# Performance work log

Hardware: AMD Instinct MI355X
Metric: run time of the kernel (lower is better)

The kernel has to match this reference:

```python
import jax, jax.numpy as jnp
import numpy as np

NUM_VARS = 64
EDGE_TYPES = 4
HID = 128
IN = 32
BATCH = 64
SKIP_FIRST = True


def setup_inputs() -> dict:
    key = jax.random.key(0)
    ks = jax.random.split(key, 16)
    adj = np.ones((NUM_VARS, NUM_VARS)) - np.eye(NUM_VARS)
    send, recv = np.where(adj)  # [N*(N-1)] each
    E = send.shape[0]
    s = 0.05
    return {
        'inputs': jax.random.normal(ks[0], (BATCH, NUM_VARS, IN), jnp.float32),
        'edges': jax.random.uniform(ks[1], (BATCH, E, EDGE_TYPES), dtype=jnp.float32),
        'msg_fc1_w': jax.random.normal(ks[2], (EDGE_TYPES, HID, 2 * IN), jnp.float32) * s,
        'msg_fc1_b': jax.random.normal(ks[3], (EDGE_TYPES, HID), jnp.float32) * s,
        'msg_fc2_w': jax.random.normal(ks[4], (EDGE_TYPES, HID, HID), jnp.float32) * s,
        'msg_fc2_b': jax.random.normal(ks[5], (EDGE_TYPES, HID), jnp.float32) * s,
        'out_fc1_w': jax.random.normal(ks[6], (HID, IN + HID), jnp.float32) * s,
        'out_fc1_b': jax.random.normal(ks[7], (HID,), jnp.float32) * s,
        'out_fc2_w': jax.random.normal(ks[8], (HID, HID), jnp.float32) * s,
        'out_fc2_b': jax.random.normal(ks[9], (HID,), jnp.float32) * s,
        'mu_w': jax.random.normal(ks[10], (IN, HID), jnp.float32) * s,
        'mu_b': jax.random.normal(ks[11], (IN,), jnp.float32) * s,
        'logstd_w': jax.random.normal(ks[12], (IN, HID), jnp.float32) * s,
        'logstd_b': jax.random.normal(ks[13], (IN,), jnp.float32) * s,
        'send_edges': jnp.asarray(send, jnp.int32),
        'recv_edges': jnp.asarray(recv, jnp.int32),
    }


def reference(inputs, edges, msg_fc1_w, msg_fc1_b, msg_fc2_w, msg_fc2_b,
              out_fc1_w, out_fc1_b, out_fc2_w, out_fc2_b,
              mu_w, mu_b, logstd_w, logstd_b, send_edges, recv_edges):
    # gather receiver/sender node features per edge: [B, E, 2*D]
    receivers = inputs[:, recv_edges, :]
    senders = inputs[:, send_edges, :]
    pre_msg = jnp.concatenate([receivers, senders], axis=-1)
    B, E, _ = pre_msg.shape
    all_msgs = jnp.zeros((B, E, HID), pre_msg.dtype)
    start = 1 if SKIP_FIRST else 0
    for i in range(start, EDGE_TYPES):  # small fixed loop over structurally distinct MLPs
        m = jax.nn.relu(jnp.einsum('bej,hj->beh', pre_msg, msg_fc1_w[i]) + msg_fc1_b[i])
        m = jax.nn.relu(jnp.einsum('beh,oh->beo', m, msg_fc2_w[i]) + msg_fc2_b[i])
        all_msgs = all_msgs + m * edges[:, :, i:i + 1]
    # scatter-add messages to receiver nodes (replaces dense one-hot matmul)
    agg_msgs = jnp.zeros((B, NUM_VARS, HID), all_msgs.dtype).at[:, recv_edges, :].add(all_msgs)
    aug_inputs = jnp.concatenate([inputs, agg_msgs], axis=-1)
    pred = jax.nn.relu(aug_inputs @ out_fc1_w.T + out_fc1_b)
    pred = jax.nn.relu(pred @ out_fc2_w.T + out_fc2_b)
    mu = pred @ mu_w.T + mu_b
    log_std = jnp.clip(pred @ logstd_w.T + logstd_b, -3.0, 1.0)
    std = jnp.exp(log_std)  # eval mode: std_gating = 0, noise suppressed
    pred_out = mu  # mu + 0 * noise * std
    return inputs + pred_out
```

## Files before the change

### kernel.cpp

```cpp
#include <hip/hip_runtime.h>
#include <hip/hip_bf16.h>

#define B_ 64
#define V_ 64
#define E_ 4032
#define HID_ 128
#define IN_ 32

typedef __attribute__((ext_vector_type(8))) __bf16 bf16x8;
typedef __attribute__((ext_vector_type(4))) __bf16 bf16x4;
typedef __attribute__((ext_vector_type(4))) float f32x4;

__global__ void __launch_bounds__(256) node_h1(
    const float* __restrict__ x, const float* __restrict__ w1,
    const float* __restrict__ b1, float* __restrict__ h1r,
    float* __restrict__ h1s) {
  const int bid = blockIdx.x, t = threadIdx.x;
  const int h = t & 127, half = t >> 7;
  __shared__ float xs[2][IN_];
  if (t < 64) xs[t >> 5][t & 31] = x[bid * 64 + t];
  __syncthreads();
#pragma unroll
  for (int tt = 0; tt < 3; ++tt) {
    const float* wrow = w1 + ((size_t)((tt + 1) * HID_ + h)) * (2 * IN_) + half * IN_;
    float4 w[8];
#pragma unroll
    for (int j = 0; j < 8; ++j) w[j] = ((const float4*)wrow)[j];
    const float bias = half ? 0.f : b1[(tt + 1) * HID_ + h];
    float* dst = (half ? h1s : h1r) + ((size_t)tt * (B_ * V_) + bid * 2) * HID_ + h;
#pragma unroll
    for (int n = 0; n < 2; ++n) {
      float acc = bias;
#pragma unroll
      for (int j = 0; j < 8; ++j)
        acc += w[j].x * xs[n][4 * j] + w[j].y * xs[n][4 * j + 1] +
               w[j].z * xs[n][4 * j + 2] + w[j].w * xs[n][4 * j + 3];
      dst[n * HID_] = acc;
    }
  }
}

__global__ void __launch_bounds__(256) weight_prep(
    const float* __restrict__ w2, const float* __restrict__ fc1w,
    const float* __restrict__ fc2w, const float* __restrict__ muw,
    unsigned short* __restrict__ w2f, float* __restrict__ fc1wT,
    float* __restrict__ fc2wT, float* __restrict__ muwT) {
  const int i = blockIdx.x * 256 + threadIdx.x;
  if (i < 49152) {
    const int e = i & 7, lane = (i >> 3) & 63, ks = (i >> 9) & 3;
    const int nt = (i >> 11) & 1, w = (i >> 12) & 3, tt = i >> 14;
    const int o = w * 32 + nt * 16 + (lane & 15);
    const int k = ks * 32 + (lane >> 4) * 8 + e;
    w2f[i] = __builtin_bit_cast(unsigned short,
                                (__bf16)w2[((size_t)((tt + 1) * HID_ + o)) * HID_ + k]);
    return;
  }
  int j = i - 49152;
  if (j < 20480) { fc1wT[j] = fc1w[(j & 127) * (IN_ + HID_) + (j >> 7)]; return; }
  j -= 20480;
  if (j < 16384) { fc2wT[j] = fc2w[(j & 127) * HID_ + (j >> 7)]; return; }
  j -= 16384;
  if (j < 4096) { muwT[j] = muw[(j & 31) * HID_ + (j >> 5)]; }
}

__global__ void __launch_bounds__(256)
edge_mfma(const float* __restrict__ edges, const float* __restrict__ b2,
          const float* __restrict__ h1r, const float* __restrict__ h1s,
          const unsigned short* __restrict__ w2f, float* __restrict__ aggout) {
  const int v = blockIdx.x, b = blockIdx.y, t = threadIdx.x;
  const int wave = t >> 6, lane = t & 63;
  const int l15 = lane & 15, lg = lane >> 4;
  const int kq = lane & 31, rpar = lane >> 5;

  __shared__ __align__(16) unsigned short m1[2][64 * HID_];
  __shared__ float ew[3 * 64];

  if (wave < 3) {
    float wgt = 0.f;
    if (lane < 63) {
      const int uu = (lane < v) ? lane : lane + 1;
      const int eg = uu * 63 + ((v > uu) ? (v - 1) : v);
      wgt = edges[(b * E_ + eg) * 4 + wave + 1];
    }
    ew[wave * 64 + lane] = wgt;
  }

  {
    float4 hr = *(const float4*)(h1r + ((size_t)b * V_ + v) * HID_ + kq * 4);
#pragma unroll
    for (int j = 0; j < 8; ++j) {
      const int r = wave * 16 + j * 2 + rpar;
      int u = (r < v) ? r : r + 1;
      if (r == 63) u = v;
      float4 hs = *(const float4*)(h1s + ((size_t)b * V_ + u) * HID_ + kq * 4);
      bf16x4 pk;
      pk[0] = (__bf16)fmaxf(hr.x + hs.x, 0.f);
      pk[1] = (__bf16)fmaxf(hr.y + hs.y, 0.f);
      pk[2] = (__bf16)fmaxf(hr.z + hs.z, 0.f);
      pk[3] = (__bf16)fmaxf(hr.w + hs.w, 0.f);
      *(bf16x4*)((char*)m1[0] + r * 256 + ((kq * 8) ^ ((r & 7) << 4))) = pk;
    }
  }

  bf16x8 bfrag[2][4];
  float b2r[2];
#pragma unroll
  for (int nt = 0; nt < 2; ++nt) {
#pragma unroll
    for (int ks = 0; ks < 4; ++ks)
      bfrag[nt][ks] = *(const bf16x8*)(w2f + (((wave * 2 + nt) * 4 + ks) * 64 + lane) * 8);
    b2r[nt] = b2[HID_ + wave * 32 + nt * 16 + l15];
  }

  float acc[4][2][4];
#pragma unroll
  for (int mt = 0; mt < 4; ++mt)
#pragma unroll
    for (int nt = 0; nt < 2; ++nt)
#pragma unroll
      for (int r = 0; r < 4; ++r) acc[mt][nt][r] = 0.f;

  __syncthreads();

#pragma unroll
  for (int tt = 0; tt < 3; ++tt) {
    float4 hrn, hsn[8];
    if (tt < 2) {
      hrn = *(const float4*)(h1r + ((size_t)((tt + 1) * B_ + b) * V_ + v) * HID_ + kq * 4);
#pragma unroll
      for (int j = 0; j < 8; ++j) {
        const int r = wave * 16 + j * 2 + rpar;
        int u = (r < v) ? r : r + 1;
        if (r == 63) u = v;
        hsn[j] = *(const float4*)(h1s + ((size_t)((tt + 1) * B_ + b) * V_ + u) * HID_ + kq * 4);
      }
    }
    const unsigned short* mb = m1[tt & 1];
#pragma unroll
    for (int mt = 0; mt < 4; ++mt) {
      bf16x8 af[4];
#pragma unroll
      for (int ks = 0; ks < 4; ++ks) {
        const int row = mt * 16 + l15;
        af[ks] = *(const bf16x8*)((const char*)mb + row * 256 +
                                  ((ks * 64 + lg * 16) ^ ((row & 7) << 4)));
      }
#pragma unroll
      for (int nt = 0; nt < 2; ++nt) {
        f32x4 macc = {0.f, 0.f, 0.f, 0.f};
#pragma unroll
        for (int ks = 0; ks < 4; ++ks)
          macc = __builtin_amdgcn_mfma_f32_16x16x32_bf16(af[ks], bfrag[nt][ks], macc, 0, 0, 0);
#pragma unroll
        for (int r = 0; r < 4; ++r)
          acc[mt][nt][r] += fmaxf(macc[r] + b2r[nt], 0.f) * ew[tt * 64 + mt * 16 + lg * 4 + r];
      }
    }
    if (tt < 2) {
#pragma unroll
      for (int j = 0; j < 8; ++j) {
        const int r = wave * 16 + j * 2 + rpar;
        bf16x4 pk;
        pk[0] = (__bf16)fmaxf(hrn.x + hsn[j].x, 0.f);
        pk[1] = (__bf16)fmaxf(hrn.y + hsn[j].y, 0.f);
        pk[2] = (__bf16)fmaxf(hrn.z + hsn[j].z, 0.f);
        pk[3] = (__bf16)fmaxf(hrn.w + hsn[j].w, 0.f);
        *(bf16x4*)((char*)m1[(tt + 1) & 1] + r * 256 + ((kq * 8) ^ ((r & 7) << 4))) = pk;
      }
#pragma unroll
      for (int nt = 0; nt < 2; ++nt) {
#pragma unroll
        for (int ks = 0; ks < 4; ++ks)
          bfrag[nt][ks] = *(const bf16x8*)(
              w2f + (((((tt + 1) * 4 + wave) * 2 + nt) * 4 + ks) * 64 + lane) * 8);
        b2r[nt] = b2[(tt + 2) * HID_ + wave * 32 + nt * 16 + l15];
      }
    }
    __syncthreads();
  }

#pragma unroll
  for (int nt = 0; nt < 2; ++nt) {
    float s = 0.f;
#pragma unroll
    for (int mt = 0; mt < 4; ++mt)
#pragma unroll
      for (int r = 0; r < 4; ++r) s += acc[mt][nt][r];
    s += __shfl_xor(s, 16);
    s += __shfl_xor(s, 32);
    if (lane < 16)
      aggout[((size_t)b * V_ + v) * HID_ + wave * 32 + nt * 16 + l15] = s;
  }
}

__global__ void __launch_bounds__(256) out_mlp(
    const float* __restrict__ x, const float* __restrict__ aggout,
    const float* __restrict__ fc1wT, const float* __restrict__ fc1b,
    const float* __restrict__ fc2wT, const float* __restrict__ fc2b,
    const float* __restrict__ muwT, const float* __restrict__ mub,
    float* __restrict__ out) {
  const int t = threadIdx.x;
  const int g = t >> 5, j = t & 31;
  const int nodebase = blockIdx.x * 8;
  __shared__ float aug[8][160];
  __shared__ float p1[8][HID_];
  __shared__ float p2[8][HID_];

  aug[t >> 5][t & 31] = x[nodebase * IN_ + t];
  {
    float4 a4 = *(const float4*)(aggout + (size_t)nodebase * HID_ + t * 4);
    *(float4*)&aug[t >> 5][IN_ + (t & 31) * 4] = a4;
  }
  __syncthreads();

  float4 a1 = *(const float4*)(fc1b + j * 4);
#pragma unroll 4
  for (int k = 0; k < IN_ + HID_; ++k) {
    float4 w = *(const float4*)(fc1wT + (size_t)k * HID_ + j * 4);
    const float a = aug[g][k];
    a1.x += w.x * a; a1.y += w.y * a; a1.z += w.z * a; a1.w += w.w * a;
  }
  a1.x = fmaxf(a1.x, 0.f); a1.y = fmaxf(a1.y, 0.f);
  a1.z = fmaxf(a1.z, 0.f); a1.w = fmaxf(a1.w, 0.f);
  *(float4*)&p1[g][j * 4] = a1;
  __syncthreads();

  float4 a2 = *(const float4*)(fc2b + j * 4);
#pragma unroll 4
  for (int k = 0; k < HID_; ++k) {
    float4 w = *(const float4*)(fc2wT + (size_t)k * HID_ + j * 4);
    const float a = p1[g][k];
    a2.x += w.x * a; a2.y += w.y * a; a2.z += w.z * a; a2.w += w.w * a;
  }
  a2.x = fmaxf(a2.x, 0.f); a2.y = fmaxf(a2.y, 0.f);
  a2.z = fmaxf(a2.z, 0.f); a2.w = fmaxf(a2.w, 0.f);
  *(float4*)&p2[g][j * 4] = a2;
  __syncthreads();

  float am = mub[j];
#pragma unroll 4
  for (int k = 0; k < HID_; ++k) am += muwT[k * IN_ + j] * p2[g][k];
  out[(size_t)(nodebase + g) * IN_ + j] = aug[g][j] + am;
}

extern "C" void kernel_launch(void* const* d_in, const int* in_sizes, int n_in,
                              void* d_out, int out_size, void* d_ws, size_t ws_size,
                              hipStream_t stream) {
  const float* x     = (const float*)d_in[0];
  const float* edges = (const float*)d_in[1];
  const float* w1    = (const float*)d_in[2];
  const float* b1    = (const float*)d_in[3];
  const float* w2    = (const float*)d_in[4];
  const float* b2    = (const float*)d_in[5];
  const float* fc1w  = (const float*)d_in[6];
  const float* fc1b  = (const float*)d_in[7];
  const float* fc2w  = (const float*)d_in[8];
  const float* fc2b  = (const float*)d_in[9];
  const float* muw   = (const float*)d_in[10];
  const float* mub   = (const float*)d_in[11];
  float* out = (float*)d_out;

  float* h1r    = (float*)d_ws;
  float* h1s    = h1r + 3 * (B_ * V_) * HID_;
  float* aggout = h1s + 3 * (B_ * V_) * HID_;
  float* fc1wT  = aggout + (B_ * V_) * HID_;
  float* fc2wT  = fc1wT + (IN_ + HID_) * HID_;
  float* muwT   = fc2wT + HID_ * HID_;
  unsigned short* w2f = (unsigned short*)(muwT + HID_ * IN_);

  node_h1<<<2048, 256, 0, stream>>>(x, w1, b1, h1r, h1s);
  weight_prep<<<352, 256, 0, stream>>>(w2, fc1w, fc2w, muw, w2f, fc1wT, fc2wT, muwT);
  edge_mfma<<<dim3(V_, B_), 256, 0, stream>>>(edges, b2, h1r, h1s, w2f, aggout);
  out_mlp<<<512, 256, 0, stream>>>(x, aggout, fc1wT, fc1b, fc2wT, fc2b, muwT, mub, out);
}
```

Before: 185.9 us.

## Store node projections in fp16, merge prep kernels, pre-transpose edge weights

Node hidden projections h1r/h1s are now stored as fp16 instead of fp32, which halves the gather traffic in the edge kernel. The relu-add is done with packed half math, and the MFMA switches from bf16 to the f16 variant. The two prep kernels are merged into one launch, which also writes a per-(b,v) transposed edge-weight table so the edge kernel does one contiguous load instead of strided gathers. The out_mlp shared arrays are padded. This trades an extra workspace buffer and fp16 range/precision risk for less memory traffic and launch overhead.

```diff
diff --git a/kernel.cpp b/kernel.cpp
--- a/kernel.cpp
+++ b/kernel.cpp
@@ -1,114 +1,132 @@
 #include <hip/hip_runtime.h>
 #include <hip/hip_bf16.h>
+#include <hip/hip_fp16.h>
 
 #define B_ 64
 #define V_ 64
 #define E_ 4032
 #define HID_ 128
 #define IN_ 32
-
-typedef __attribute__((ext_vector_type(8))) __bf16 bf16x8;
-typedef __attribute__((ext_vector_type(4))) __bf16 bf16x4;
+#define BV_ (B_ * V_)
+
+typedef __attribute__((ext_vector_type(2))) _Float16 f16x2;
+typedef __attribute__((ext_vector_type(8))) _Float16 f16x8;
 typedef __attribute__((ext_vector_type(4))) float f32x4;
 
-__global__ void __launch_bounds__(256) node_h1(
+__device__ __forceinline__ f16x2 bc2(unsigned u) { return __builtin_bit_cast(f16x2, u); }
+__device__ __forceinline__ unsigned bcu(f16x2 h) { return __builtin_bit_cast(unsigned, h); }
+
+__global__ void __launch_bounds__(256) prep_all(
     const float* __restrict__ x, const float* __restrict__ w1,
-    const float* __restrict__ b1, float* __restrict__ h1r,
-    float* __restrict__ h1s) {
+    const float* __restrict__ b1, const float* __restrict__ w2,
+    const float* __restrict__ edges, const float* __restrict__ fc1w,
+    const float* __restrict__ fc2w, const float* __restrict__ muw,
+    _Float16* __restrict__ h1r, _Float16* __restrict__ h1s,
+    _Float16* __restrict__ w2f, float* __restrict__ ewT,
+    float* __restrict__ fc1wT, float* __restrict__ fc2wT,
+    float* __restrict__ muwT) {
   const int bid = blockIdx.x, t = threadIdx.x;
-  const int h = t & 127, half = t >> 7;
-  __shared__ float xs[2][IN_];
-  if (t < 64) xs[t >> 5][t & 31] = x[bid * 64 + t];
-  __syncthreads();
-#pragma unroll
-  for (int tt = 0; tt < 3; ++tt) {
-    const float* wrow = w1 + ((size_t)((tt + 1) * HID_ + h)) * (2 * IN_) + half * IN_;
-    float4 w[8];
-#pragma unroll
-    for (int j = 0; j < 8; ++j) w[j] = ((const float4*)wrow)[j];
-    const float bias = half ? 0.f : b1[(tt + 1) * HID_ + h];
-    float* dst = (half ? h1s : h1r) + ((size_t)tt * (B_ * V_) + bid * 2) * HID_ + h;
-#pragma unroll
-    for (int n = 0; n < 2; ++n) {
-      float acc = bias;
-#pragma unroll
-      for (int j = 0; j < 8; ++j)
-        acc += w[j].x * xs[n][4 * j] + w[j].y * xs[n][4 * j + 1] +
-               w[j].z * xs[n][4 * j + 2] + w[j].w * xs[n][4 * j + 3];
-      dst[n * HID_] = acc;
-    }
-  }
-}
-
-__global__ void __launch_bounds__(256) weight_prep(
-    const float* __restrict__ w2, const float* __restrict__ fc1w,
-    const float* __restrict__ fc2w, const float* __restrict__ muw,
-    unsigned short* __restrict__ w2f, float* __restrict__ fc1wT,
-    float* __restrict__ fc2wT, float* __restrict__ muwT) {
-  const int i = blockIdx.x * 256 + threadIdx.x;
-  if (i < 49152) {
+
+  if (bid < 2048) {
+    __shared__ float xs[2][IN_];
+    if (t < 64) xs[t >> 5][t & 31] = x[bid * 64 + t];
+    __syncthreads();
+    const int h = t & 127, half_ = t >> 7;
+#pragma unroll
+    for (int tt = 0; tt < 3; ++tt) {
+      const float* wrow = w1 + ((size_t)((tt + 1) * HID_ + h)) * (2 * IN_) + half_ * IN_;
+      float4 w[8];
+#pragma unroll
+      for (int j = 0; j < 8; ++j) w[j] = ((const float4*)wrow)[j];
+      const float bias = half_ ? 0.f : b1[(tt + 1) * HID_ + h];
+      _Float16* dst = (half_ ? h1s : h1r) + ((size_t)tt * BV_ + bid * 2) * HID_ + h;
+#pragma unroll
+      for (int n = 0; n < 2; ++n) {
+        float acc = bias;
+#pragma unroll
+        for (int j = 0; j < 8; ++j)
+          acc += w[j].x * xs[n][4 * j] + w[j].y * xs[n][4 * j + 1] +
+                 w[j].z * xs[n][4 * j + 2] + w[j].w * xs[n][4 * j + 3];
+        dst[n * HID_] = (_Float16)acc;
+      }
+    }
+    return;
+  }
+  if (bid < 2240) {
+    const int i = (bid - 2048) * 256 + t;
     const int e = i & 7, lane = (i >> 3) & 63, ks = (i >> 9) & 3;
     const int nt = (i >> 11) & 1, w = (i >> 12) & 3, tt = i >> 14;
     const int o = w * 32 + nt * 16 + (lane & 15);
     const int k = ks * 32 + (lane >> 4) * 8 + e;
-    w2f[i] = __builtin_bit_cast(unsigned short,
-                                (__bf16)w2[((size_t)((tt + 1) * HID_ + o)) * HID_ + k]);
-    return;
-  }
-  int j = i - 49152;
-  if (j < 20480) { fc1wT[j] = fc1w[(j & 127) * (IN_ + HID_) + (j >> 7)]; return; }
-  j -= 20480;
-  if (j < 16384) { fc2wT[j] = fc2w[(j & 127) * HID_ + (j >> 7)]; return; }
-  j -= 16384;
-  if (j < 4096) { muwT[j] = muw[(j & 31) * HID_ + (j >> 5)]; }
+    w2f[i] = (_Float16)w2[((size_t)((tt + 1) * HID_ + o)) * HID_ + k];
+    return;
+  }
+  if (bid < 2400) {
+    int j = (bid - 2240) * 256 + t;
+    if (j < 20480) { fc1wT[j] = fc1w[(j & 127) * (IN_ + HID_) + (j >> 7)]; return; }
+    j -= 20480;
+    if (j < 16384) { fc2wT[j] = fc2w[(j & 127) * HID_ + (j >> 7)]; return; }
+    j -= 16384;
+    muwT[j] = muw[(j & 31) * HID_ + (j >> 5)];
+    return;
+  }
+  {
+    const int g = bid - 2400;
+    if (t < 192) {
+      const int b = g >> 6, v = g & 63;
+      const int tt = t >> 6, r = t & 63;
+      float val = 0.f;
+      if (r < 63) {
+        const int u = (r < v) ? r : r + 1;
+        const int vv = (v > u) ? v - 1 : v;
+        val = edges[((size_t)b * E_ + u * 63 + vv) * 4 + tt + 1];
+      }
+      ewT[(size_t)g * 192 + t] = val;
+    }
+    return;
+  }
 }
 
 __global__ void __launch_bounds__(256)
-edge_mfma(const float* __restrict__ edges, const float* __restrict__ b2,
-          const float* __restrict__ h1r, const float* __restrict__ h1s,
-          const unsigned short* __restrict__ w2f, float* __restrict__ aggout) {
+edge_mfma(const float* __restrict__ b2, const _Float16* __restrict__ h1r,
+          const _Float16* __restrict__ h1s, const _Float16* __restrict__ w2f,
+          const float* __restrict__ ewT, float* __restrict__ aggout) {
   const int v = blockIdx.x, b = blockIdx.y, t = threadIdx.x;
   const int wave = t >> 6, lane = t & 63;
   const int l15 = lane & 15, lg = lane >> 4;
   const int kq = lane & 31, rpar = lane >> 5;
 
   __shared__ __align__(16) unsigned short m1[2][64 * HID_];
-  __shared__ float ew[3 * 64];
-
-  if (wave < 3) {
-    float wgt = 0.f;
-    if (lane < 63) {
-      const int uu = (lane < v) ? lane : lane + 1;
-      const int eg = uu * 63 + ((v > uu) ? (v - 1) : v);
-      wgt = edges[(b * E_ + eg) * 4 + wave + 1];
-    }
-    ew[wave * 64 + lane] = wgt;
-  }
+  __shared__ __align__(16) float ews[192];
+
+  if (t < 192) ews[t] = ewT[((size_t)b * V_ + v) * 192 + t];
 
   {
-    float4 hr = *(const float4*)(h1r + ((size_t)b * V_ + v) * HID_ + kq * 4);
+    const unsigned short* hrp =
+        (const unsigned short*)h1r + ((size_t)b * V_ + v) * HID_ + kq * 4;
+    uint2 hru = *(const uint2*)hrp;
+    const f16x2 hr0 = bc2(hru.x), hr1 = bc2(hru.y);
 #pragma unroll
     for (int j = 0; j < 8; ++j) {
       const int r = wave * 16 + j * 2 + rpar;
       int u = (r < v) ? r : r + 1;
       if (r == 63) u = v;
-      float4 hs = *(const float4*)(h1s + ((size_t)b * V_ + u) * HID_ + kq * 4);
-      bf16x4 pk;
-      pk[0] = (__bf16)fmaxf(hr.x + hs.x, 0.f);
-      pk[1] = (__bf16)fmaxf(hr.y + hs.y, 0.f);
-      pk[2] = (__bf16)fmaxf(hr.z + hs.z, 0.f);
-      pk[3] = (__bf16)fmaxf(hr.w + hs.w, 0.f);
-      *(bf16x4*)((char*)m1[0] + r * 256 + ((kq * 8) ^ ((r & 7) << 4))) = pk;
-    }
-  }
-
-  bf16x8 bfrag[2][4];
+      uint2 hsu = *(const uint2*)((const unsigned short*)h1s +
+                                  ((size_t)b * V_ + u) * HID_ + kq * 4);
+      f16x2 o0 = __builtin_elementwise_max(hr0 + bc2(hsu.x), (f16x2)0);
+      f16x2 o1 = __builtin_elementwise_max(hr1 + bc2(hsu.y), (f16x2)0);
+      uint2 pk = {bcu(o0), bcu(o1)};
+      *(uint2*)((char*)m1[0] + r * 256 + ((kq * 8) ^ ((r & 7) << 4))) = pk;
+    }
+  }
+
+  f16x8 bfrag[2][4];
   float b2r[2];
 #pragma unroll
   for (int nt = 0; nt < 2; ++nt) {
 #pragma unroll
     for (int ks = 0; ks < 4; ++ks)
-      bfrag[nt][ks] = *(const bf16x8*)(w2f + (((wave * 2 + nt) * 4 + ks) * 64 + lane) * 8);
+      bfrag[nt][ks] = *(const f16x8*)(w2f + (((wave * 2 + nt) * 4 + ks) * 64 + lane) * 8);
     b2r[nt] = b2[HID_ + wave * 32 + nt * 16 + l15];
   }
 
@@ -124,54 +142,57 @@
 
 #pragma unroll
   for (int tt = 0; tt < 3; ++tt) {
-    float4 hrn, hsn[8];
+    uint2 hrn, hsn[8];
     if (tt < 2) {
-      hrn = *(const float4*)(h1r + ((size_t)((tt + 1) * B_ + b) * V_ + v) * HID_ + kq * 4);
+      hrn = *(const uint2*)((const unsigned short*)h1r +
+                            ((size_t)((tt + 1) * B_ + b) * V_ + v) * HID_ + kq * 4);
 #pragma unroll
       for (int j = 0; j < 8; ++j) {
         const int r = wave * 16 + j * 2 + rpar;
         int u = (r < v) ? r : r + 1;
         if (r == 63) u = v;
-        hsn[j] = *(const float4*)(h1s + ((size_t)((tt + 1) * B_ + b) * V_ + u) * HID_ + kq * 4);
+        hsn[j] = *(const uint2*)((const unsigned short*)h1s +
+                                 ((size_t)((tt + 1) * B_ + b) * V_ + u) * HID_ + kq * 4);
       }
     }
     const unsigned short* mb = m1[tt & 1];
 #pragma unroll
     for (int mt = 0; mt < 4; ++mt) {
-      bf16x8 af[4];
+      f16x8 af[4];
 #pragma unroll
       for (int ks = 0; ks < 4; ++ks) {
         const int row = mt * 16 + l15;
-        af[ks] = *(const bf16x8*)((const char*)mb + row * 256 +
-                                  ((ks * 64 + lg * 16) ^ ((row & 7) << 4)));
-      }
+        af[ks] = *(const f16x8*)((const char*)mb + row * 256 +
+                                 ((ks * 64 + lg * 16) ^ ((row & 7) << 4)));
+      }
+      const float4 ew4 = *(const float4*)&ews[tt * 64 + mt * 16 + lg * 4];
 #pragma unroll
       for (int nt = 0; nt < 2; ++nt) {
         f32x4 macc = {0.f, 0.f, 0.f, 0.f};
 #pragma unroll
         for (int ks = 0; ks < 4; ++ks)
-          macc = __builtin_amdgcn_mfma_f32_16x16x32_bf16(af[ks], bfrag[nt][ks], macc, 0, 0, 0);
-#pragma unroll
-        for (int r = 0; r < 4; ++r)
-          acc[mt][nt][r] += fmaxf(macc[r] + b2r[nt], 0.f) * ew[tt * 64 + mt * 16 + lg * 4 + r];
+          macc = __builtin_amdgcn_mfma_f32_16x16x32_f16(af[ks], bfrag[nt][ks], macc, 0, 0, 0);
+        acc[mt][nt][0] += fmaxf(macc[0] + b2r[nt], 0.f) * ew4.x;
+        acc[mt][nt][1] += fmaxf(macc[1] + b2r[nt], 0.f) * ew4.y;
+        acc[mt][nt][2] += fmaxf(macc[2] + b2r[nt], 0.f) * ew4.z;
+        acc[mt][nt][3] += fmaxf(macc[3] + b2r[nt], 0.f) * ew4.w;
       }
     }
     if (tt < 2) {
+      const f16x2 hr0 = bc2(hrn.x), hr1 = bc2(hrn.y);
 #pragma unroll
       for (int j = 0; j < 8; ++j) {
         const int r = wave * 16 + j * 2 + rpar;
-        bf16x4 pk;
-        pk[0] = (__bf16)fmaxf(hrn.x + hsn[j].x, 0.f);
-        pk[1] = (__bf16)fmaxf(hrn.y + hsn[j].y, 0.f);
-        pk[2] = (__bf16)fmaxf(hrn.z + hsn[j].z, 0.f);
-        pk[3] = (__bf16)fmaxf(hrn.w + hsn[j].w, 0.f);
-        *(bf16x4*)((char*)m1[(tt + 1) & 1] + r * 256 + ((kq * 8) ^ ((r & 7) << 4))) = pk;
+        f16x2 o0 = __builtin_elementwise_max(hr0 + bc2(hsn[j].x), (f16x2)0);
+        f16x2 o1 = __builtin_elementwise_max(hr1 + bc2(hsn[j].y), (f16x2)0);
+        uint2 pk = {bcu(o0), bcu(o1)};
+        *(uint2*)((char*)m1[(tt + 1) & 1] + r * 256 + ((kq * 8) ^ ((r & 7) << 4))) = pk;
       }
 #pragma unroll
       for (int nt = 0; nt < 2; ++nt) {
 #pragma unroll
         for (int ks = 0; ks < 4; ++ks)
-          bfrag[nt][ks] = *(const bf16x8*)(
+          bfrag[nt][ks] = *(const f16x8*)(
               w2f + (((((tt + 1) * 4 + wave) * 2 + nt) * 4 + ks) * 64 + lane) * 8);
         b2r[nt] = b2[(tt + 2) * HID_ + wave * 32 + nt * 16 + l15];
       }
@@ -202,9 +223,9 @@
   const int t = threadIdx.x;
   const int g = t >> 5, j = t & 31;
   const int nodebase = blockIdx.x * 8;
-  __shared__ float aug[8][160];
-  __shared__ float p1[8][HID_];
-  __shared__ float p2[8][HID_];
+  __shared__ __align__(16) float aug[8][164];
+  __shared__ __align__(16) float p1[8][132];
+  __shared__ __align__(16) float p2[8][132];
 
   aug[t >> 5][t & 31] = x[nodebase * IN_ + t];
   {
@@ -260,16 +281,17 @@
   const float* mub   = (const float*)d_in[11];
   float* out = (float*)d_out;
 
-  float* h1r    = (float*)d_ws;
-  float* h1s    = h1r + 3 * (B_ * V_) * HID_;
-  float* aggout = h1s + 3 * (B_ * V_) * HID_;
-  float* fc1wT  = aggout + (B_ * V_) * HID_;
+  float* aggout = (float*)d_ws;
+  float* fc1wT  = aggout + BV_ * HID_;
   float* fc2wT  = fc1wT + (IN_ + HID_) * HID_;
   float* muwT   = fc2wT + HID_ * HID_;
-  unsigned short* w2f = (unsigned short*)(muwT + HID_ * IN_);
-
-  node_h1<<<2048, 256, 0, stream>>>(x, w1, b1, h1r, h1s);
-  weight_prep<<<352, 256, 0, stream>>>(w2, fc1w, fc2w, muw, w2f, fc1wT, fc2wT, muwT);
-  edge_mfma<<<dim3(V_, B_), 256, 0, stream>>>(edges, b2, h1r, h1s, w2f, aggout);
+  float* ewT    = muwT + HID_ * IN_;
+  _Float16* h1r = (_Float16*)(ewT + (size_t)BV_ * 192);
+  _Float16* h1s = h1r + (size_t)3 * BV_ * HID_;
+  _Float16* w2f = h1s + (size_t)3 * BV_ * HID_;
+
+  prep_all<<<6496, 256, 0, stream>>>(x, w1, b1, w2, edges, fc1w, fc2w, muw,
+                                     h1r, h1s, w2f, ewT, fc1wT, fc2wT, muwT);
+  edge_mfma<<<dim3(V_, B_), 256, 0, stream>>>(b2, h1r, h1s, w2f, ewT, aggout);
   out_mlp<<<512, 256, 0, stream>>>(x, aggout, fc1wT, fc1b, fc2wT, fc2b, muwT, mub, out);
 }
```

New measurement: 183.3 us. About the same (-1.4%).
